# Optimization experiments

Hardware: AMD Instinct MI355X
Metric: run time of the kernel (lower is better)

The kernel has to match this reference:

```python
import jax, jax.numpy as jnp
import numpy as np
from jax import lax

N_GRAPHS = 256
N_NODES = 128      # nodes per graph (fixed-size batching)
N_TPLT = 16
N_TPLT_NODES = 10
N_FEAT = 128
AVG_DEG = 8
EPS = 0.1          # entropic regularization for the GW solver
OUTER_ITERS = 5    # outer mirror-descent (entropic GW) iterations
SINKHORN_ITERS = 20


def setup_inputs() -> dict:
    key = jax.random.key(0)
    k1, k2, k3, k4, k5 = jax.random.split(key, 5)
    x = jax.random.normal(k1, (N_GRAPHS * N_NODES, N_FEAT), jnp.float32)
    # per-graph random edges with global node ids (PyG convention)
    n_e = N_NODES * AVG_DEG
    src = jax.random.randint(k2, (N_GRAPHS, n_e), 0, N_NODES)
    dst = jax.random.randint(k3, (N_GRAPHS, n_e), 0, N_NODES)
    off = (jnp.arange(N_GRAPHS) * N_NODES)[:, None]
    edge_index = jnp.stack([(src + off).reshape(-1), (dst + off).reshape(-1)]).astype(jnp.int32)
    batch = jnp.repeat(jnp.arange(N_GRAPHS, dtype=jnp.int32), N_NODES)
    # template parameters (symmetric uniform adjacencies, normal features, zero q0 -> uniform weights)
    A0 = jax.random.uniform(k4, (N_TPLT, N_TPLT_NODES, N_TPLT_NODES), jnp.float32)
    tplt_adjacencies = 0.5 * (A0 + jnp.swapaxes(A0, 1, 2))
    tplt_features = jax.random.normal(k5, (N_TPLT, N_TPLT_NODES, N_FEAT), jnp.float32)
    q0 = jnp.zeros((N_TPLT, N_TPLT_NODES), jnp.float32)
    return {"x": x, "edge_index": edge_index, "batch": batch,
            "tplt_adjacencies": tplt_adjacencies, "tplt_features": tplt_features, "q0": q0}


def _gw_distances(C1, C2, p, q):
    # C1: [B,N,N] graph adjacencies, C2: [T,M,M] templates, p: [N], q: [T,M]
    # square-loss GW decomposition (Peyre et al.): f1=a^2, f2=b^2, h1=a, h2=2b
    B, N = C1.shape[0], C1.shape[1]
    T, M = C2.shape[0], C2.shape[1]
    f1p = jnp.einsum('bij,j->bi', C1 * C1, p)          # [B,N]
    f2q = jnp.einsum('tij,tj->ti', C2 * C2, q)         # [T,M]
    constC = f1p[:, None, :, None] + f2q[None, :, None, :]  # [B,T,N,M]

    def tens(P):
        # constC - h1(C1) P h2(C2)^T
        cross = jnp.einsum('bik,btkm,tjm->btij', C1, P, 2.0 * C2)
        return constC - cross

    P0 = jnp.broadcast_to(p[None, None, :, None] * q[None, :, None, :], (B, T, N, M))

    def outer(P, _):
        cost = 2.0 * tens(P)                     # GW gradient
        K = jnp.exp(-cost / EPS)                 # [B,T,N,M]
        u0 = jnp.ones((B, T, N), K.dtype)
        v0 = jnp.ones((B, T, M), K.dtype)

        def inner(carry, _):
            u, v = carry
            u = p[None, None, :] / jnp.einsum('btnm,btm->btn', K, v)
            v = q[None, :, :] / jnp.einsum('btnm,btn->btm', K, u)
            return (u, v), None

        (u, v), _ = lax.scan(inner, (u0, v0), None, length=SINKHORN_ITERS)
        P = u[..., :, None] * K * v[..., None, :]
        return P, None

    P, _ = lax.scan(outer, P0, None, length=OUTER_ITERS)
    return jnp.sum(tens(P) * P, axis=(2, 3))     # [B,T]


def reference(x, edge_index, batch, tplt_adjacencies, tplt_features, q0):
    # q = softmax(q0, dim=1): template node weights
    q = jax.nn.softmax(q0, axis=1)
    # dense per-graph adjacency from the sparse edge list
    g = batch[edge_index[0]]
    src = edge_index[0] - g * N_NODES
    dst = edge_index[1] - g * N_NODES
    C1 = jnp.zeros((N_GRAPHS, N_NODES, N_NODES), x.dtype)
    C1 = C1.at[g, src, dst].set(1.0)
    C1 = jnp.maximum(C1, jnp.swapaxes(C1, 1, 2))  # undirected
    p = jnp.full((N_NODES,), 1.0 / N_NODES, x.dtype)  # uniform graph node weights
    # fused=False: pure Gromov-Wasserstein, node features are not used
    return _gw_distances(C1, tplt_adjacencies, p, q)
```

## Files before the change

### kernel.cpp

```cpp
#include <hip/hip_runtime.h>

#define NGRAPH 256
#define NN     128
#define NT     16
#define NM     10
#define OUTER_IT 5
#define SINK_IT  20

#define SC1  28.85390081777927f
#define SC2  57.70780163555854f

typedef unsigned long long u64;
typedef float v2f __attribute__((ext_vector_type(2)));
typedef float v4f __attribute__((ext_vector_type(4)));
typedef _Float16 h2 __attribute__((ext_vector_type(2)));

static __device__ __forceinline__ v2f pkfma(v2f a, v2f b, v2f c) {
  return __builtin_elementwise_fma(a, b, c);
}
static __device__ __forceinline__ v2f bc2(float s) { return (v2f){s, s}; }
static __device__ __forceinline__ h2 u2h(unsigned u) { h2 r; __builtin_memcpy(&r, &u, 4); return r; }
static __device__ __forceinline__ unsigned pkrtz(float x, float y) {
  auto h = __builtin_amdgcn_cvt_pkrtz(x, y);
  unsigned r; __builtin_memcpy(&r, &h, 4); return r;
}

template <int CTRL>
__device__ __forceinline__ float dpp_add(float a) {
  int t = __builtin_amdgcn_update_dpp(0, __float_as_int(a), CTRL, 0xf, 0xf, true);
  return a + __int_as_float(t);
}
__device__ __forceinline__ float allsum32(float x) {
  x = dpp_add<0xB1>(x);
  x = dpp_add<0x4E>(x);
  x = dpp_add<0x141>(x);
  x = dpp_add<0x140>(x);
  int sw = __builtin_amdgcn_ds_swizzle(__float_as_int(x), 0x401F);
  return x + __int_as_float(sw);
}

__global__ __launch_bounds__(64, 2)
void tgw_kernel(const int* __restrict__ ei,
                const float* __restrict__ tadj,
                const float* __restrict__ q0g,
                float* __restrict__ out,
                int E, int ne) {
  const int lane = threadIdx.x;
  const int p    = lane >> 5;
  const int sub  = lane & 31;
  const int b    = blockIdx.x >> 3;
  const int t0   = (blockIdx.x & 7) * 2;

  __shared__ __align__(16) unsigned adj[NN][4];
  __shared__ __align__(16) unsigned Pf[2][NN][6];
  __shared__ __align__(16) v2f C2T[2][NM][6];
  __shared__ float q0s[2][NM];

  for (int i = lane; i < NN * 4; i += 64) (&adj[0][0])[i] = 0u;
  for (int i = lane; i < 2 * NM * 5; i += 64) {
    int tt = i / 50, r = i % 50, m = r / 5, jp = r % 5;
    const float* bp = tadj + (t0 + tt) * NM * NM + m;
    C2T[tt][m][jp] = (v2f){bp[(2 * jp) * NM], bp[(2 * jp + 1) * NM]} * SC2;
  }
  if (lane < 2 * NM) q0s[lane / NM][lane % NM] = q0g[t0 * NM + lane];
  __syncthreads();

  const int* srcp = ei;
  const int* dstp = ei + E;
  const int ebase = b * ne;
  for (int e = lane; e < ne; e += 64) {
    int s = srcp[ebase + e] & (NN - 1);
    int d = dstp[ebase + e] & (NN - 1);
    atomicOr(&adj[s][d >> 5], 1u << (d & 31));
    atomicOr(&adj[d][s >> 5], 1u << (s & 31));
  }
  __syncthreads();

  float qv[NM];
  {
    float mx = q0s[p][0];
    #pragma unroll
    for (int j = 1; j < NM; ++j) mx = fmaxf(mx, q0s[p][j]);
    float s = 0.f;
    #pragma unroll
    for (int j = 0; j < NM; ++j) { qv[j] = __expf(q0s[p][j] - mx); s += qv[j]; }
    float inv = __builtin_amdgcn_rcpf(s);
    #pragma unroll
    for (int j = 0; j < NM; ++j) qv[j] *= inv;
  }
  v2f q2[5];
  #pragma unroll
  for (int jp = 0; jp < 5; ++jp) q2[jp] = (v2f){qv[2 * jp], qv[2 * jp + 1]};

  v2f fq2[5], qC2T[5];
  {
    #pragma unroll
    for (int jp = 0; jp < 5; ++jp) { fq2[jp] = (v2f){0.f, 0.f}; qC2T[jp] = (v2f){0.f, 0.f}; }
    #pragma unroll
    for (int m = 0; m < NM; ++m) {
      v2f qb = bc2(qv[m]);
      #pragma unroll
      for (int jp = 0; jp < 5; ++jp) {
        v2f c = C2T[p][m][jp];
        fq2[jp]  = pkfma(c * c, qb, fq2[jp]);
        qC2T[jp] = pkfma(c, qb, qC2T[jp]);
      }
    }
    const float f = -1.0f / (4.0f * SC1);
    #pragma unroll
    for (int jp = 0; jp < 5; ++jp) fq2[jp] *= f;
  }

  const float pw = 1.0f / 128.0f;
  float f1p[4], m1f1[4];
  #pragma unroll
  for (int c = 0; c < 4; ++c) {
    uint4 mm = *(const uint4*)&adj[sub + 32 * c][0];
    u64 m0 = mm.x | ((u64)mm.y << 32), m1 = mm.z | ((u64)mm.w << 32);
    f1p[c]  = (float)(__popcll(m0) + __popcll(m1)) * pw;
    m1f1[c] = -SC1 * f1p[c];
  }

  const unsigned* Pbase = &Pf[p][0][0];
  auto gatherRow = [&](int r, v2f* S2) {
    uint4 mm = *(const uint4*)&adj[r][0];
    u64 m0 = mm.x | ((u64)mm.y << 32), m1 = mm.z | ((u64)mm.w << 32);
    h2 S[5] = {};
    #pragma unroll
    for (int half = 0; half < 2; ++half) {
      u64 m = half ? m1 : m0;
      const int kb = half ? 64 : 0;
      while (m) {
        int k1 = kb + (int)__builtin_ctzll(m); m &= m - 1;
        const unsigned* r1 = Pbase + k1 * 6;
        uint2 a1 = *(const uint2*)r1;
        uint2 b1 = *(const uint2*)(r1 + 2);
        unsigned c1 = r1[4];
        if (m) {
          int k2 = kb + (int)__builtin_ctzll(m); m &= m - 1;
          const unsigned* r2 = Pbase + k2 * 6;
          uint2 a2 = *(const uint2*)r2;
          uint2 b2 = *(const uint2*)(r2 + 2);
          unsigned c2 = r2[4];
          S[0] += u2h(a1.x); S[1] += u2h(a1.y); S[2] += u2h(b1.x);
          S[3] += u2h(b1.y); S[4] += u2h(c1);
          S[0] += u2h(a2.x); S[1] += u2h(a2.y); S[2] += u2h(b2.x);
          S[3] += u2h(b2.y); S[4] += u2h(c2);
        } else {
          S[0] += u2h(a1.x); S[1] += u2h(a1.y); S[2] += u2h(b1.x);
          S[3] += u2h(b1.y); S[4] += u2h(c1);
        }
      }
    }
    #pragma unroll
    for (int h = 0; h < 5; ++h) S2[h] = (v2f){(float)S[h].x, (float)S[h].y};
  };

  auto costFromS = [&](v2f Sm[4][5], v2f arg2[4][5]) {
    #pragma unroll
    for (int c = 0; c < 4; ++c)
      #pragma unroll
      for (int jp = 0; jp < 5; ++jp) arg2[c][jp] = fq2[jp] + bc2(m1f1[c]);
    #pragma unroll
    for (int m = 0; m < NM; ++m) {
      v4f X = *(const v4f*)&C2T[p][m][0];
      v4f Y = *(const v4f*)&C2T[p][m][2];
      v2f Z = *(const v2f*)&C2T[p][m][4];
      #pragma unroll
      for (int c = 0; c < 4; ++c) {
        float sv = (m & 1) ? Sm[c][m >> 1].y : Sm[c][m >> 1].x;
        v2f sb = bc2(sv);
        arg2[c][0] = pkfma(sb, X.xy, arg2[c][0]);
        arg2[c][1] = pkfma(sb, X.zw, arg2[c][1]);
        arg2[c][2] = pkfma(sb, Y.xy, arg2[c][2]);
        arg2[c][3] = pkfma(sb, Y.zw, arg2[c][3]);
        arg2[c][4] = pkfma(sb, Z,    arg2[c][4]);
      }
    }
  };

  v2f K2[4][5], v2[5], arg2[4][5];
  float uu[4];

  for (int o = 0; o < OUTER_IT; ++o) {
    if (o == 0) {
      #pragma unroll
      for (int c = 0; c < 4; ++c) {
        v2f fb = bc2(f1p[c]);
        v2f ob = bc2(m1f1[c]);
        #pragma unroll
        for (int jp = 0; jp < 5; ++jp)
          arg2[c][jp] = pkfma(fb, qC2T[jp], fq2[jp] + ob);
      }
    } else {
      v2f Sm[4][5];
      #pragma unroll
      for (int c = 0; c < 4; ++c) gatherRow(sub + 32 * c, Sm[c]);
      costFromS(Sm, arg2);
    }
    #pragma unroll
    for (int c = 0; c < 4; ++c)
      #pragma unroll
      for (int jp = 0; jp < 5; ++jp)
        K2[c][jp] = (v2f){exp2f(arg2[c][jp].x), exp2f(arg2[c][jp].y)};

    #pragma unroll
    for (int jp = 0; jp < 5; ++jp) v2[jp] = (v2f){1.f, 1.f};
    for (int it = 0; it < SINK_IT; ++it) {
      #pragma unroll
      for (int c = 0; c < 4; ++c) {
        v2f d2 = K2[c][0] * v2[0];
        d2 = pkfma(K2[c][1], v2[1], d2);
        d2 = pkfma(K2[c][2], v2[2], d2);
        d2 = pkfma(K2[c][3], v2[3], d2);
        d2 = pkfma(K2[c][4], v2[4], d2);
        uu[c] = pw * __builtin_amdgcn_rcpf(d2.x + d2.y);
      }
      #pragma unroll
      for (int jp = 0; jp < 5; ++jp) {
        v2f w2 = K2[0][jp] * bc2(uu[0]);
        w2 = pkfma(K2[1][jp], bc2(uu[1]), w2);
        w2 = pkfma(K2[2][jp], bc2(uu[2]), w2);
        w2 = pkfma(K2[3][jp], bc2(uu[3]), w2);
        float cx = allsum32(w2.x);
        float cy = allsum32(w2.y);
        v2[jp] = (v2f){q2[jp].x * __builtin_amdgcn_rcpf(cx),
                       q2[jp].y * __builtin_amdgcn_rcpf(cy)};
      }
    }

    __syncthreads();
    #pragma unroll
    for (int c = 0; c < 4; ++c) {
      v2f ub = bc2(uu[c]);
      v2f x0 = K2[c][0] * ub * v2[0];
      v2f x1 = K2[c][1] * ub * v2[1];
      v2f x2 = K2[c][2] * ub * v2[2];
      v2f x3 = K2[c][3] * ub * v2[3];
      v2f x4 = K2[c][4] * ub * v2[4];
      unsigned* row = &Pf[p][sub + 32 * c][0];
      uint2 w01 = {pkrtz(x0.x, x0.y), pkrtz(x1.x, x1.y)};
      uint2 w23 = {pkrtz(x2.x, x2.y), pkrtz(x3.x, x3.y)};
      *(uint2*)row       = w01;
      *(uint2*)(row + 2) = w23;
      row[4]             = pkrtz(x4.x, x4.y);
    }
    __syncthreads();
  }

  float acc = 0.f;
  {
    v2f Sm[4][5];
    #pragma unroll
    for (int c = 0; c < 4; ++c) gatherRow(sub + 32 * c, Sm[c]);
    costFromS(Sm, arg2);
    const v2f nf = bc2(-1.0f / SC1);
    v2f acc2 = (v2f){0.f, 0.f};
    #pragma unroll
    for (int c = 0; c < 4; ++c) {
      v2f ub = bc2(uu[c]);
      #pragma unroll
      for (int jp = 0; jp < 5; ++jp) {
        v2f Pv = K2[c][jp] * ub * v2[jp];
        acc2 = pkfma(arg2[c][jp] * nf, Pv, acc2);
      }
    }
    acc = acc2.x + acc2.y;
  }
  float total = allsum32(acc);
  if (sub == 0) out[b * NT + t0 + p] = total;
}

extern "C" void kernel_launch(void* const* d_in, const int* in_sizes, int n_in,
                              void* d_out, int out_size, void* d_ws, size_t ws_size,
                              hipStream_t stream) {
  const int* ei   = (const int*)d_in[1];
  const float* c2 = (const float*)d_in[3];
  const float* q0 = (const float*)d_in[5];
  float* out      = (float*)d_out;
  const int E  = in_sizes[1] / 2;
  const int ne = E / NGRAPH;
  tgw_kernel<<<dim3(NGRAPH * 8), dim3(64), 0, stream>>>(ei, c2, q0, out, E, ne);
}
```

Before: 207.7 us.

## Compute adjacency-times-transport product with MFMA instead of sparse gather

```diff
diff --git a/kernel.cpp b/kernel.cpp
--- a/kernel.cpp
+++ b/kernel.cpp
@@ -13,17 +13,12 @@
 typedef unsigned long long u64;
 typedef float v2f __attribute__((ext_vector_type(2)));
 typedef float v4f __attribute__((ext_vector_type(4)));
-typedef _Float16 h2 __attribute__((ext_vector_type(2)));
+typedef _Float16 half8 __attribute__((ext_vector_type(8)));
 
 static __device__ __forceinline__ v2f pkfma(v2f a, v2f b, v2f c) {
   return __builtin_elementwise_fma(a, b, c);
 }
 static __device__ __forceinline__ v2f bc2(float s) { return (v2f){s, s}; }
-static __device__ __forceinline__ h2 u2h(unsigned u) { h2 r; __builtin_memcpy(&r, &u, 4); return r; }
-static __device__ __forceinline__ unsigned pkrtz(float x, float y) {
-  auto h = __builtin_amdgcn_cvt_pkrtz(x, y);
-  unsigned r; __builtin_memcpy(&r, &h, 4); return r;
-}
 
 template <int CTRL>
 __device__ __forceinline__ float dpp_add(float a) {
@@ -48,11 +43,14 @@
   const int lane = threadIdx.x;
   const int p    = lane >> 5;
   const int sub  = lane & 31;
+  const int mrow = lane & 15;
+  const int quad = lane >> 4;
   const int b    = blockIdx.x >> 3;
   const int t0   = (blockIdx.x & 7) * 2;
 
   __shared__ __align__(16) unsigned adj[NN][4];
-  __shared__ __align__(16) unsigned Pf[2][NN][6];
+  __shared__ __align__(16) _Float16 Pt[2][16][136];
+  __shared__ __align__(16) float Srow[2][NN][12];
   __shared__ __align__(16) v2f C2T[2][NM][6];
   __shared__ float q0s[2][NM];
 
@@ -92,18 +90,17 @@
   #pragma unroll
   for (int jp = 0; jp < 5; ++jp) q2[jp] = (v2f){qv[2 * jp], qv[2 * jp + 1]};
 
-  v2f fq2[5], qC2T[5];
+  v2f fq2[5];
   {
     #pragma unroll
-    for (int jp = 0; jp < 5; ++jp) { fq2[jp] = (v2f){0.f, 0.f}; qC2T[jp] = (v2f){0.f, 0.f}; }
+    for (int jp = 0; jp < 5; ++jp) fq2[jp] = (v2f){0.f, 0.f};
     #pragma unroll
     for (int m = 0; m < NM; ++m) {
       v2f qb = bc2(qv[m]);
       #pragma unroll
       for (int jp = 0; jp < 5; ++jp) {
         v2f c = C2T[p][m][jp];
-        fq2[jp]  = pkfma(c * c, qb, fq2[jp]);
-        qC2T[jp] = pkfma(c, qb, qC2T[jp]);
+        fq2[jp] = pkfma(c * c, qb, fq2[jp]);
       }
     }
     const float f = -1.0f / (4.0f * SC1);
@@ -121,39 +118,50 @@
     m1f1[c] = -SC1 * f1p[c];
   }
 
-  const unsigned* Pbase = &Pf[p][0][0];
-  auto gatherRow = [&](int r, v2f* S2) {
-    uint4 mm = *(const uint4*)&adj[r][0];
-    u64 m0 = mm.x | ((u64)mm.y << 32), m1 = mm.z | ((u64)mm.w << 32);
-    h2 S[5] = {};
-    #pragma unroll
-    for (int half = 0; half < 2; ++half) {
-      u64 m = half ? m1 : m0;
-      const int kb = half ? 64 : 0;
-      while (m) {
-        int k1 = kb + (int)__builtin_ctzll(m); m &= m - 1;
-        const unsigned* r1 = Pbase + k1 * 6;
-        uint2 a1 = *(const uint2*)r1;
-        uint2 b1 = *(const uint2*)(r1 + 2);
-        unsigned c1 = r1[4];
-        if (m) {
-          int k2 = kb + (int)__builtin_ctzll(m); m &= m - 1;
-          const unsigned* r2 = Pbase + k2 * 6;
-          uint2 a2 = *(const uint2*)r2;
-          uint2 b2 = *(const uint2*)(r2 + 2);
-          unsigned c2 = r2[4];
-          S[0] += u2h(a1.x); S[1] += u2h(a1.y); S[2] += u2h(b1.x);
-          S[3] += u2h(b1.y); S[4] += u2h(c1);
-          S[0] += u2h(a2.x); S[1] += u2h(a2.y); S[2] += u2h(b2.x);
-          S[3] += u2h(b2.y); S[4] += u2h(c2);
-        } else {
-          S[0] += u2h(a1.x); S[1] += u2h(a1.y); S[2] += u2h(b1.x);
-          S[3] += u2h(b1.y); S[4] += u2h(c1);
+  half8 Afrag[8][4];
+  #pragma unroll
+  for (int Mt = 0; Mt < 8; ++Mt) {
+    #pragma unroll
+    for (int Kt = 0; Kt < 4; ++Kt) {
+      unsigned w  = adj[Mt * 16 + mrow][Kt];
+      unsigned by = (w >> (quad * 8)) & 0xFFu;
+      union { unsigned u[4]; half8 h; } cv;
+      #pragma unroll
+      for (int t = 0; t < 4; ++t) {
+        unsigned b0 = (by >> (2 * t)) & 1u;
+        unsigned b1 = (by >> (2 * t + 1)) & 1u;
+        cv.u[t] = (b0 ? 0x3C00u : 0u) | (b1 ? 0x3C000000u : 0u);
+      }
+      Afrag[Mt][Kt] = cv.h;
+    }
+  }
+
+  auto mfmaPass = [&]() {
+    #pragma unroll
+    for (int pp = 0; pp < 2; ++pp) {
+      v4f acc[8];
+      #pragma unroll
+      for (int Mt = 0; Mt < 8; ++Mt) acc[Mt] = (v4f){0.f, 0.f, 0.f, 0.f};
+      #pragma unroll
+      for (int Kt = 0; Kt < 4; ++Kt) {
+        half8 bf = *(const half8*)&Pt[pp][mrow][Kt * 32 + quad * 8];
+        #pragma unroll
+        for (int Mt = 0; Mt < 8; ++Mt)
+          acc[Mt] = __builtin_amdgcn_mfma_f32_16x16x32_f16(
+              Afrag[Mt][Kt], bf, acc[Mt], 0, 0, 0);
+      }
+      if (mrow < NM) {
+        #pragma unroll
+        for (int Mt = 0; Mt < 8; ++Mt) {
+          int mb = Mt * 16 + quad * 4;
+          Srow[pp][mb + 0][mrow] = acc[Mt].x;
+          Srow[pp][mb + 1][mrow] = acc[Mt].y;
+          Srow[pp][mb + 2][mrow] = acc[Mt].z;
+          Srow[pp][mb + 3][mrow] = acc[Mt].w;
         }
       }
     }
-    #pragma unroll
-    for (int h = 0; h < 5; ++h) S2[h] = (v2f){(float)S[h].x, (float)S[h].y};
+    __syncthreads();
   };
 
   auto costFromS = [&](v2f Sm[4][5], v2f arg2[4][5]) {
@@ -178,26 +186,32 @@
       }
     }
   };
+  auto loadS = [&](v2f Sm[4][5]) {
+    #pragma unroll
+    for (int c = 0; c < 4; ++c) {
+      const float* sr = &Srow[p][sub + 32 * c][0];
+      v4f A = *(const v4f*)sr;
+      v4f B = *(const v4f*)(sr + 4);
+      v2f C = *(const v2f*)(sr + 8);
+      Sm[c][0] = A.xy; Sm[c][1] = A.zw; Sm[c][2] = B.xy; Sm[c][3] = B.zw; Sm[c][4] = C;
+    }
+  };
 
   v2f K2[4][5], v2[5], arg2[4][5];
   float uu[4];
 
   for (int o = 0; o < OUTER_IT; ++o) {
+    v2f Sm[4][5];
     if (o == 0) {
       #pragma unroll
-      for (int c = 0; c < 4; ++c) {
-        v2f fb = bc2(f1p[c]);
-        v2f ob = bc2(m1f1[c]);
+      for (int c = 0; c < 4; ++c)
         #pragma unroll
-        for (int jp = 0; jp < 5; ++jp)
-          arg2[c][jp] = pkfma(fb, qC2T[jp], fq2[jp] + ob);
-      }
+        for (int h = 0; h < 5; ++h) Sm[c][h] = bc2(f1p[c]) * q2[h];
     } else {
-      v2f Sm[4][5];
-      #pragma unroll
-      for (int c = 0; c < 4; ++c) gatherRow(sub + 32 * c, Sm[c]);
-      costFromS(Sm, arg2);
-    }
+      mfmaPass();
+      loadS(Sm);
+    }
+    costFromS(Sm, arg2);
     #pragma unroll
     for (int c = 0; c < 4; ++c)
       #pragma unroll
@@ -232,18 +246,18 @@
     __syncthreads();
     #pragma unroll
     for (int c = 0; c < 4; ++c) {
+      const int k = sub + 32 * c;
       v2f ub = bc2(uu[c]);
       v2f x0 = K2[c][0] * ub * v2[0];
       v2f x1 = K2[c][1] * ub * v2[1];
       v2f x2 = K2[c][2] * ub * v2[2];
       v2f x3 = K2[c][3] * ub * v2[3];
       v2f x4 = K2[c][4] * ub * v2[4];
-      unsigned* row = &Pf[p][sub + 32 * c][0];
-      uint2 w01 = {pkrtz(x0.x, x0.y), pkrtz(x1.x, x1.y)};
-      uint2 w23 = {pkrtz(x2.x, x2.y), pkrtz(x3.x, x3.y)};
-      *(uint2*)row       = w01;
-      *(uint2*)(row + 2) = w23;
-      row[4]             = pkrtz(x4.x, x4.y);
+      Pt[p][0][k] = (_Float16)x0.x; Pt[p][1][k] = (_Float16)x0.y;
+      Pt[p][2][k] = (_Float16)x1.x; Pt[p][3][k] = (_Float16)x1.y;
+      Pt[p][4][k] = (_Float16)x2.x; Pt[p][5][k] = (_Float16)x2.y;
+      Pt[p][6][k] = (_Float16)x3.x; Pt[p][7][k] = (_Float16)x3.y;
+      Pt[p][8][k] = (_Float16)x4.x; Pt[p][9][k] = (_Float16)x4.y;
     }
     __syncthreads();
   }
@@ -251,8 +265,8 @@
   float acc = 0.f;
   {
     v2f Sm[4][5];
-    #pragma unroll
-    for (int c = 0; c < 4; ++c) gatherRow(sub + 32 * c, Sm[c]);
+    mfmaPass();
+    loadS(Sm);
     costFromS(Sm, arg2);
     const v2f nf = bc2(-1.0f / SC1);
     v2f acc2 = (v2f){0.f, 0.f};
```

Result: slower. 275.4 us (+32.6%).
